# Optimization experiments

Measured on AMD Instinct MI355X. Metric: run time of the kernel, lower is better.

The kernel has to match this reference:

```python
import jax, jax.numpy as jnp
import numpy as np

NEG_SLOPE = 0.2  # PyG GATConv default


def gat_layer(x, W, att_src, att_dst, bias, src, dst, concat):
    # x: [N, F_in]; W: [F_in, H*C]; att_src/att_dst: [H, C]; bias: [H*C] or [C]
    N = x.shape[0]
    H, C = att_src.shape
    h = (x @ W).reshape(N, H, C)                       # [N, H, C]
    a_s = jnp.einsum('nhc,hc->nh', h, att_src)         # [N, H]
    a_d = jnp.einsum('nhc,hc->nh', h, att_dst)
    e = jax.nn.leaky_relu(a_s[src] + a_d[dst], NEG_SLOPE)  # [E, H]
    # segment softmax over incoming edges of each destination node
    m = jax.ops.segment_max(e, dst, num_segments=N)
    m = jnp.where(jnp.isfinite(m), m, 0.0)
    ee = jnp.exp(e - m[dst])
    s = jax.ops.segment_sum(ee, dst, num_segments=N)
    alpha = ee / (s[dst] + 1e-16)                      # [E, H]
    out = jax.ops.segment_sum(h[src] * alpha[:, :, None], dst, num_segments=N)  # [N, H, C]
    out = out.reshape(N, H * C) if concat else out.mean(axis=1)
    return out + bias


def setup_inputs() -> dict:
    key = jax.random.key(0)
    ks = jax.random.split(key, 16)
    N, E, F_IN, NC = 100000, 3200000, 256, 40
    H, C = 8, 8  # hidden GATConv: heads=8, out=8 -> width 64
    inp = {}
    inp['features'] = jax.random.normal(ks[0], (N, F_IN), dtype=jnp.float32)
    inp['edge_index'] = jax.random.randint(ks[1], (2, E), 0, N, dtype=jnp.int64)
    def p(k, shape):
        return jax.random.normal(k, shape, dtype=jnp.float32) * 0.1
    # layer 0: in 256 -> 8 heads x 8 (concat -> 64)
    inp['W0'] = p(ks[2], (F_IN, H * C)); inp['as0'] = p(ks[3], (H, C)); inp['ad0'] = p(ks[4], (H, C)); inp['b0'] = jnp.zeros((H * C,), jnp.float32)
    # layer 1: 64 -> 8 heads x 8 (concat -> 64)
    inp['W1'] = p(ks[5], (H * C, H * C)); inp['as1'] = p(ks[6], (H, C)); inp['ad1'] = p(ks[7], (H, C)); inp['b1'] = jnp.zeros((H * C,), jnp.float32)
    # layer 2: 64 -> 1 head x n_classes (mean/no-concat)
    inp['W2'] = p(ks[8], (H * C, NC)); inp['as2'] = p(ks[9], (1, NC)); inp['ad2'] = p(ks[10], (1, NC)); inp['b2'] = jnp.zeros((NC,), jnp.float32)
    return inp


def reference(features, edge_index, W0, as0, ad0, b0, W1, as1, ad1, b1, W2, as2, ad2, b2):
    N = features.shape[0]
    loops = jnp.arange(N, dtype=edge_index.dtype)  # PyG GATConv adds self-loops by default
    src = jnp.concatenate([edge_index[0], loops])
    dst = jnp.concatenate([edge_index[1], loops])
    x = gat_layer(features, W0, as0, ad0, b0, src, dst, True)
    x = gat_layer(x, W1, as1, ad1, b1, src, dst, True)
    x = gat_layer(x, W2, as2, ad2, b2, src, dst, False)
    return jax.nn.log_softmax(x, axis=-1)
```

## Files before the change

kernel.cpp:

```cpp
#include <hip/hip_runtime.h>
#include <hip/hip_bf16.h>

#define NEG_SLOPE 0.2f
#define LOG2E 1.44269504f
#define EPB 4096

typedef __attribute__((ext_vector_type(8))) short short8;
typedef __attribute__((ext_vector_type(4))) float f32x4;

__device__ __forceinline__ unsigned short f2bf(float x) {
    unsigned u = __float_as_uint(x);
    unsigned r = (u + 0x7FFFu + ((u >> 16) & 1u)) >> 16;
    return (unsigned short)r;
}

__device__ __forceinline__ float fexp2(float x) {
    return __builtin_amdgcn_exp2f(x);
}

__device__ __forceinline__ float readlane_f(float v, int l) {
    return __int_as_float(__builtin_amdgcn_readlane(__float_as_int(v), l));
}


__global__ __launch_bounds__(256) void bucket_hist_k(
    const int* __restrict__ dsts, int* __restrict__ bcnt, int E, int Etot,
    int nbuck) {
    __shared__ int lh[512];
    for (int i = threadIdx.x; i < nbuck; i += 256) lh[i] = 0;
    __syncthreads();
    int base = blockIdx.x * EPB;
    int cnt = Etot - base;
    if (cnt > EPB) cnt = EPB;
    for (int i = threadIdx.x; i < cnt; i += 256) {
        int e = base + i;
        int d = (e < E) ? dsts[e] : (e - E);
        atomicAdd(&lh[d >> 8], 1);
    }
    __syncthreads();
    for (int i = threadIdx.x; i < nbuck; i += 256) {
        int c = lh[i];
        if (c) atomicAdd(&bcnt[i], c);
    }
}

__global__ __launch_bounds__(512) void bucket_scan_k(
    const int* __restrict__ bcnt, int* __restrict__ bptr,
    int* __restrict__ bcur, int nbuck, int Etot) {
    __shared__ int tmp[512];
    int t = threadIdx.x;
    int v = (t < nbuck) ? bcnt[t] : 0;
    tmp[t] = v;
    __syncthreads();
    for (int off = 1; off < 512; off <<= 1) {
        int x = (t >= off) ? tmp[t - off] : 0;
        __syncthreads();
        tmp[t] += x;
        __syncthreads();
    }
    int excl = tmp[t] - v;
    if (t < nbuck) { bptr[t] = excl; bcur[t] = excl; }
    if (t == 0) bptr[nbuck] = Etot;
}

__global__ __launch_bounds__(256) void bucket_scatter_k(
    const int* __restrict__ srcs, const int* __restrict__ dsts,
    int* __restrict__ bcur, int2* __restrict__ pairs, int E, int Etot,
    int nbuck) {
    __shared__ int lh[512];
    __shared__ int lbase[512];
    for (int i = threadIdx.x; i < nbuck; i += 256) lh[i] = 0;
    __syncthreads();
    int base = blockIdx.x * EPB;
    int cnt = Etot - base;
    if (cnt > EPB) cnt = EPB;
    for (int i = threadIdx.x; i < cnt; i += 256) {
        int e = base + i;
        int d = (e < E) ? dsts[e] : (e - E);
        atomicAdd(&lh[d >> 8], 1);
    }
    __syncthreads();
    for (int i = threadIdx.x; i < nbuck; i += 256) {
        int c = lh[i];
        lbase[i] = c ? atomicAdd(&bcur[i], c) : 0;
    }
    __syncthreads();
    for (int i = threadIdx.x; i < nbuck; i += 256) lh[i] = 0;
    __syncthreads();
    for (int i = threadIdx.x; i < cnt; i += 256) {
        int e = base + i;
        int s, d;
        if (e < E) { s = srcs[e]; d = dsts[e]; }
        else       { s = e - E;   d = s; }
        int b = d >> 8;
        int off = atomicAdd(&lh[b], 1);
        pairs[lbase[b] + off] = make_int2(s, d);
    }
}

__global__ __launch_bounds__(256) void bucket_sort_k(
    const int2* __restrict__ pairs, const int* __restrict__ bptr,
    int* __restrict__ row_ptr, int* __restrict__ csr_src, int N, int Etot,
    int nbuck) {
    __shared__ int lh[256];
    __shared__ int lscan[256];
    int b = blockIdx.x;
    int n0 = b << 8;
    int e0 = bptr[b], e1 = bptr[b + 1];
    int t = threadIdx.x;
    lh[t] = 0;
    __syncthreads();
    for (int e = e0 + t; e < e1; e += 256)
        atomicAdd(&lh[pairs[e].y - n0], 1);
    __syncthreads();
    int v = lh[t];
    lscan[t] = v;
    __syncthreads();
    for (int off = 1; off < 256; off <<= 1) {
        int x = (t >= off) ? lscan[t - off] : 0;
        __syncthreads();
        lscan[t] += x;
        __syncthreads();
    }
    int start = e0 + lscan[t] - v;
    int n = n0 + t;
    if (n < N) row_ptr[n] = start;
    lh[t] = start;
    __syncthreads();
    for (int e = e0 + t; e < e1; e += 256) {
        int2 p = pairs[e];
        int pos = atomicAdd(&lh[p.y - n0], 1);
        csr_src[pos] = p.x;
    }
    if (b == nbuck - 1 && t == 0) row_ptr[N] = Etot;
}


template <int K>
__global__ __launch_bounds__(256) void gemm_pack8_k(
    const float* __restrict__ x, const float* __restrict__ W,
    const float* __restrict__ a_src, const float* __restrict__ a_dst,
    char* __restrict__ hrec, float* __restrict__ asb,
    float* __restrict__ adb, int N) {
    constexpr int NT = 4;
    constexpr int KT = K / 32;
    constexpr size_t WF_BYTES = (size_t)KT * NT * 64 * 8 * sizeof(short);
    constexpr size_t H_BYTES = (size_t)64 * 65 * sizeof(float);
    __shared__ alignas(16) char smem[WF_BYTES > H_BYTES ? WF_BYTES : H_BYTES];
    short* Wf = (short*)smem;
    float* hL = (float*)smem;
    int tid = threadIdx.x;
    for (int f = tid; f < KT * NT * 64; f += 256) {
        int lane = f & 63;
        int ntk = f >> 6;
        int nt = ntk % NT, kt = ntk / NT;
        int q = lane >> 4, c = lane & 15;
        int n = nt * 16 + c;
        int k0 = kt * 32 + q * 8;
        short8 frag;
        #pragma unroll
        for (int j = 0; j < 8; ++j)
            frag[j] = (short)f2bf(W[(size_t)(k0 + j) * 64 + n]);
        *(short8*)&Wf[f * 8] = frag;
    }
    __syncthreads();
    int wave = tid >> 6, lane = tid & 63;
    int q = lane >> 4, c = lane & 15;
    int m0 = blockIdx.x * 64 + wave * 16;
    int arow = m0 + c;
    int arl = arow < N ? arow : N - 1;
    f32x4 acc[NT] = {};
    for (int kt = 0; kt < KT; ++kt) {
        const float* xp = x + (size_t)arl * K + kt * 32 + q * 8;
        float4 a0 = *(const float4*)xp;
        float4 a1 = *(const float4*)(xp + 4);
        float av[8] = {a0.x, a0.y, a0.z, a0.w, a1.x, a1.y, a1.z, a1.w};
        short8 af;
        #pragma unroll
        for (int j = 0; j < 8; ++j) af[j] = (short)f2bf(av[j]);
        #pragma unroll
        for (int nt = 0; nt < NT; ++nt) {
            short8 bf = *(const short8*)&Wf[((kt * NT + nt) * 64 + lane) * 8];
            acc[nt] = __builtin_amdgcn_mfma_f32_16x16x32_bf16(af, bf, acc[nt],
                                                              0, 0, 0);
        }
    }
    __syncthreads();
    int lrow = wave * 16 + q * 4;
    #pragma unroll
    for (int nt = 0; nt < NT; ++nt)
        #pragma unroll
        for (int reg = 0; reg < 4; ++reg)
            hL[(lrow + reg) * 65 + nt * 16 + c] = acc[nt][reg];
    __syncthreads();
    #pragma unroll
    for (int it = 0; it < 2; ++it) {
        int id = it * 256 + tid;
        int ln = id >> 3, hd = id & 7;
        int gn = blockIdx.x * 64 + ln;
        if (gn >= N) continue;
        const float* hp = &hL[ln * 65 + hd * 8];
        float as = 0.f, ad = 0.f;
        float hv[8];
        #pragma unroll
        for (int j = 0; j < 8; ++j) {
            hv[j] = hp[j];
            as += hv[j] * a_src[hd * 8 + j];
            ad += hv[j] * a_dst[hd * 8 + j];
        }
        adb[gn * 8 + hd] = ad * LOG2E;
        asb[gn * 8 + hd] = as * LOG2E;
        unsigned short u[8];
        #pragma unroll
        for (int j = 0; j < 8; ++j) u[j] = f2bf(hv[j]);
        uint4 pk;
        pk.x = (unsigned)u[0] | ((unsigned)u[1] << 16);
        pk.y = (unsigned)u[2] | ((unsigned)u[3] << 16);
        pk.z = (unsigned)u[4] | ((unsigned)u[5] << 16);
        pk.w = (unsigned)u[6] | ((unsigned)u[7] << 16);
        *(uint4*)(hrec + (size_t)gn * 128 + hd * 16) = pk;
    }
}


__global__ __launch_bounds__(256) void gemm_pack40_k(
    const float* __restrict__ x, const float* __restrict__ W,
    const float* __restrict__ a_src, const float* __restrict__ a_dst,
    char* __restrict__ h40, float* __restrict__ asb40,
    float* __restrict__ adb, int N) {
    constexpr int K = 64, NT = 3, KT = 2;
    constexpr size_t WF_BYTES = (size_t)KT * NT * 64 * 8 * sizeof(short);
    constexpr size_t H_BYTES = (size_t)64 * 41 * sizeof(float);
    __shared__ alignas(16) char smem[WF_BYTES > H_BYTES ? WF_BYTES : H_BYTES];
    short* Wf = (short*)smem;
    float* hL = (float*)smem;
    int tid = threadIdx.x;
    for (int f = tid; f < KT * NT * 64; f += 256) {
        int lane = f & 63;
        int ntk = f >> 6;
        int nt = ntk % NT, kt = ntk / NT;
        int q = lane >> 4, c = lane & 15;
        int n = nt * 16 + c;
        int k0 = kt * 32 + q * 8;
        short8 frag;
        #pragma unroll
        for (int j = 0; j < 8; ++j) {
            float v = (n < 40) ? W[(size_t)(k0 + j) * 40 + n] : 0.f;
            frag[j] = (short)f2bf(v);
        }
        *(short8*)&Wf[f * 8] = frag;
    }
    __syncthreads();
    int wave = tid >> 6, lane = tid & 63;
    int q = lane >> 4, c = lane & 15;
    int m0 = blockIdx.x * 64 + wave * 16;
    int arow = m0 + c;
    int arl = arow < N ? arow : N - 1;
    f32x4 acc[NT] = {};
    for (int kt = 0; kt < KT; ++kt) {
        const float* xp = x + (size_t)arl * K + kt * 32 + q * 8;
        float4 a0 = *(const float4*)xp;
        float4 a1 = *(const float4*)(xp + 4);
        float av[8] = {a0.x, a0.y, a0.z, a0.w, a1.x, a1.y, a1.z, a1.w};
        short8 af;
        #pragma unroll
        for (int j = 0; j < 8; ++j) af[j] = (short)f2bf(av[j]);
        #pragma unroll
        for (int nt = 0; nt < NT; ++nt) {
            short8 bf = *(const short8*)&Wf[((kt * NT + nt) * 64 + lane) * 8];
            acc[nt] = __builtin_amdgcn_mfma_f32_16x16x32_bf16(af, bf, acc[nt],
                                                              0, 0, 0);
        }
    }
    __syncthreads();
    int lrow = wave * 16 + q * 4;
    #pragma unroll
    for (int nt = 0; nt < NT; ++nt) {
        int n = nt * 16 + c;
        if (n >= 40) continue;
        #pragma unroll
        for (int reg = 0; reg < 4; ++reg)
            hL[(lrow + reg) * 41 + n] = acc[nt][reg];
    }
    __syncthreads();
    int ln = tid >> 2, sub = tid & 3;
    int gn = blockIdx.x * 64 + ln;
    float pas = 0.f, pad = 0.f;
    if (gn < N) {
        for (int j = sub; j < 40; j += 4) {
            float hv = hL[ln * 41 + j];
            pas += hv * a_src[j];
            pad += hv * a_dst[j];
        }
    }
    pas += __shfl_xor(pas, 1); pas += __shfl_xor(pas, 2);
    pad += __shfl_xor(pad, 1); pad += __shfl_xor(pad, 2);
    if (gn < N && sub == 0) {
        asb40[gn] = pas * LOG2E;
        adb[gn] = pad * LOG2E;
    }
    for (int i = tid; i < 64 * 40; i += 256) {
        int n2 = i / 40, ch = i % 40;
        int g2 = blockIdx.x * 64 + n2;
        if (g2 < N)
            *(unsigned short*)(h40 + (size_t)g2 * 80 + ch * 2) =
                f2bf(hL[n2 * 41 + ch]);
    }
}


#define EDGE64(SUF, IDX)                                                     \
    int s##SUF = __builtin_amdgcn_readlane(sv, (IDX));                       \
    float w##SUF = lwp[(IDX)];                                               \
    unsigned u##SUF =                                                        \
        *(const unsigned short*)(hrec + (size_t)s##SUF * 128 + lane2);

__global__ __launch_bounds__(256) void aggr64_k(
    const char* __restrict__ hrec, const float* __restrict__ asb,
    const float* __restrict__ adb, const int* __restrict__ row_ptr,
    const int* __restrict__ csr_src, const float* __restrict__ bias,
    float* __restrict__ out, int N) {
    __shared__ float wlds[4 * 1040];
    int wave = threadIdx.x >> 6;
    int node = blockIdx.x * 4 + wave;
    if (node >= N) return;
    int lane = threadIdx.x & 63;
    int hd = lane >> 3;
    int lane2 = lane * 2;
    float* wbA = wlds + wave * 1040;
    float* wbB = wbA + 520;
    const float* lwpA = wbA + hd * 65;
    const float* lwpB = wbB + hd * 65;
    int beg = row_ptr[node], end = row_ptr[node + 1];
    float4 adv0 = *(const float4*)(adb + (size_t)node * 8);
    float4 adv1 = *(const float4*)(adb + (size_t)node * 8 + 4);
    float acc0 = 0.f, acc1 = 0.f, acc2 = 0.f, acc3 = 0.f;
    float acc4 = 0.f, acc5 = 0.f, acc6 = 0.f, acc7 = 0.f;
    float l0 = 0.f, l1 = 0.f, l2 = 0.f, l3 = 0.f;
    float l4 = 0.f, l5 = 0.f, l6 = 0.f, l7 = 0.f;
    int par = 0;
    for (int i0 = beg; i0 < end; i0 += 64, par ^= 1) {
        int tail = end - i0;
        int sv = csr_src[i0 + (lane < tail ? lane : 0)];
        int cnt = tail < 64 ? tail : 64;
        float* wb = par ? wbB : wbA;
        const float* lwp = par ? lwpB : lwpA;
        {
            const float* asp = asb + (size_t)sv * 8;
            float4 s0 = *(const float4*)asp;
            float4 s1 = *(const float4*)(asp + 4);
            float w0 = s0.x + adv0.x; w0 = fmaxf(w0, NEG_SLOPE * w0); w0 = fexp2(w0);
            float w1 = s0.y + adv0.y; w1 = fmaxf(w1, NEG_SLOPE * w1); w1 = fexp2(w1);
            float w2 = s0.z + adv0.z; w2 = fmaxf(w2, NEG_SLOPE * w2); w2 = fexp2(w2);
            float w3 = s0.w + adv0.w; w3 = fmaxf(w3, NEG_SLOPE * w3); w3 = fexp2(w3);
            float w4 = s1.x + adv1.x; w4 = fmaxf(w4, NEG_SLOPE * w4); w4 = fexp2(w4);
            float w5 = s1.y + adv1.y; w5 = fmaxf(w5, NEG_SLOPE * w5); w5 = fexp2(w5);
            float w6 = s1.z + adv1.z; w6 = fmaxf(w6, NEG_SLOPE * w6); w6 = fexp2(w6);
            float w7 = s1.w + adv1.w; w7 = fmaxf(w7, NEG_SLOPE * w7); w7 = fexp2(w7);
            wb[lane]       = w0;
            wb[65 + lane]  = w1;
            wb[130 + lane] = w2;
            wb[195 + lane] = w3;
            wb[260 + lane] = w4;
            wb[325 + lane] = w5;
            wb[390 + lane] = w6;
            wb[455 + lane] = w7;
        }
        int j = 0;
        for (; j + 8 <= cnt; j += 8) {
            EDGE64(A, j)      EDGE64(B, j + 1) EDGE64(C, j + 2) EDGE64(D, j + 3)
            EDGE64(E2, j + 4) EDGE64(F, j + 5) EDGE64(G, j + 6) EDGE64(H2, j + 7)
            l0 += wA; l1 += wB; l2 += wC; l3 += wD;
            l4 += wE2; l5 += wF; l6 += wG; l7 += wH2;
            acc0 = fmaf(wA, __uint_as_float(uA << 16), acc0);
            acc1 = fmaf(wB, __uint_as_float(uB << 16), acc1);
            acc2 = fmaf(wC, __uint_as_float(uC << 16), acc2);
            acc3 = fmaf(wD, __uint_as_float(uD << 16), acc3);
            acc4 = fmaf(wE2, __uint_as_float(uE2 << 16), acc4);
            acc5 = fmaf(wF, __uint_as_float(uF << 16), acc5);
            acc6 = fmaf(wG, __uint_as_float(uG << 16), acc6);
            acc7 = fmaf(wH2, __uint_as_float(uH2 << 16), acc7);
        }
        for (; j + 4 <= cnt; j += 4) {
            EDGE64(A, j) EDGE64(B, j + 1) EDGE64(C, j + 2) EDGE64(D, j + 3)
            l0 += wA; l1 += wB; l2 += wC; l3 += wD;
            acc0 = fmaf(wA, __uint_as_float(uA << 16), acc0);
            acc1 = fmaf(wB, __uint_as_float(uB << 16), acc1);
            acc2 = fmaf(wC, __uint_as_float(uC << 16), acc2);
            acc3 = fmaf(wD, __uint_as_float(uD << 16), acc3);
        }
        for (; j < cnt; ++j) {
            EDGE64(A, j)
            l0 += wA;
            acc0 = fmaf(wA, __uint_as_float(uA << 16), acc0);
        }
    }
    float l = ((l0 + l1) + (l2 + l3)) + ((l4 + l5) + (l6 + l7));
    float acc = ((acc0 + acc1) + (acc2 + acc3)) + ((acc4 + acc5) + (acc6 + acc7));
    out[(size_t)node * 64 + lane] = acc / (l + 1e-16f) + bias[lane];
}


#define F40(SUF, IDX)                                                        \
    int s##SUF = __builtin_amdgcn_readlane(sv, (IDX));                       \
    float w##SUF = readlane_f(wv, (IDX));                                    \
    unsigned u##SUF =                                                        \
        *(const unsigned short*)(hrec + (size_t)s##SUF * 80 + cl2);

__global__ __launch_bounds__(256) void aggr40_k(
    const char* __restrict__ hrec, const float* __restrict__ asb,
    const float* __restrict__ adb, const int* __restrict__ row_ptr,
    const int* __restrict__ csr_src, const float* __restrict__ bias,
    float* __restrict__ out, int N) {
    int node = blockIdx.x * 4 + (threadIdx.x >> 6);
    if (node >= N) return;
    int lane = threadIdx.x & 63;
    int cl2 = (lane < 40 ? lane : 0) * 2;
    int beg = row_ptr[node], end = row_ptr[node + 1];
    float ad = adb[node];
    float acc0 = 0.f, acc1 = 0.f, acc2 = 0.f, acc3 = 0.f;
    float acc4 = 0.f, acc5 = 0.f, acc6 = 0.f, acc7 = 0.f;
    float lpart = 0.f;
    for (int i0 = beg; i0 < end; i0 += 64) {
        int tail = end - i0;
        int sv = csr_src[i0 + (lane < tail ? lane : 0)];
        int cnt = tail < 64 ? tail : 64;
        float as = asb[sv];
        float v = as + ad;
        v = fmaxf(v, NEG_SLOPE * v);
        float wv = fexp2(v);
        wv = (lane < cnt) ? wv : 0.f;
        lpart += wv;
        int j = 0;
        for (; j + 8 <= cnt; j += 8) {
            F40(A, j)     F40(B, j + 1) F40(C, j + 2) F40(D, j + 3)
            F40(E2, j + 4) F40(F, j + 5) F40(G, j + 6) F40(H2, j + 7)
            acc0 = fmaf(wA, __uint_as_float(uA << 16), acc0);
            acc1 = fmaf(wB, __uint_as_float(uB << 16), acc1);
            acc2 = fmaf(wC, __uint_as_float(uC << 16), acc2);
            acc3 = fmaf(wD, __uint_as_float(uD << 16), acc3);
            acc4 = fmaf(wE2, __uint_as_float(uE2 << 16), acc4);
            acc5 = fmaf(wF, __uint_as_float(uF << 16), acc5);
            acc6 = fmaf(wG, __uint_as_float(uG << 16), acc6);
            acc7 = fmaf(wH2, __uint_as_float(uH2 << 16), acc7);
        }
        for (; j + 4 <= cnt; j += 4) {
            F40(A, j) F40(B, j + 1) F40(C, j + 2) F40(D, j + 3)
            acc0 = fmaf(wA, __uint_as_float(uA << 16), acc0);
            acc1 = fmaf(wB, __uint_as_float(uB << 16), acc1);
            acc2 = fmaf(wC, __uint_as_float(uC << 16), acc2);
            acc3 = fmaf(wD, __uint_as_float(uD << 16), acc3);
        }
        for (; j < cnt; ++j) {
            F40(A, j)
            acc0 = fmaf(wA, __uint_as_float(uA << 16), acc0);
        }
    }
    #pragma unroll
    for (int off = 32; off > 0; off >>= 1) lpart += __shfl_xor(lpart, off);
    float l = lpart;
    float acc = ((acc0 + acc1) + (acc2 + acc3)) + ((acc4 + acc5) + (acc6 + acc7));
    float val = acc / (l + 1e-16f) + ((lane < 40) ? bias[lane] : 0.f);
    float mval = (lane < 40) ? val : -1e30f;
    #pragma unroll
    for (int off = 32; off > 0; off >>= 1)
        mval = fmaxf(mval, __shfl_xor(mval, off));
    float ex = (lane < 40) ? __expf(val - mval) : 0.f;
    #pragma unroll
    for (int off = 32; off > 0; off >>= 1) ex += __shfl_xor(ex, off);
    if (lane < 40)
        out[(size_t)node * 40 + lane] = val - mval - __logf(ex);
}


extern "C" void kernel_launch(void* const* d_in, const int* in_sizes, int n_in,
                              void* d_out, int out_size, void* d_ws,
                              size_t ws_size, hipStream_t stream) {
    const float* features = (const float*)d_in[0];
    const int* edge_index = (const int*)d_in[1];
    const float* W0 = (const float*)d_in[2];
    const float* as0 = (const float*)d_in[3];
    const float* ad0 = (const float*)d_in[4];
    const float* b0 = (const float*)d_in[5];
    const float* W1 = (const float*)d_in[6];
    const float* as1 = (const float*)d_in[7];
    const float* ad1 = (const float*)d_in[8];
    const float* b1 = (const float*)d_in[9];
    const float* W2 = (const float*)d_in[10];
    const float* as2 = (const float*)d_in[11];
    const float* ad2 = (const float*)d_in[12];
    const float* b2 = (const float*)d_in[13];

    int N = in_sizes[0] / 256;
    int E = in_sizes[1] / 2;
    int Etot = E + N;
    int nbuck = (N + 255) >> 8;
    const int* srcs = edge_index;
    const int* dsts = edge_index + E;

    float* ws = (float*)d_ws;
    float* Hbuf = ws;
    float* Abuf = Hbuf + (size_t)N * 64;
    float* adb  = Abuf + (size_t)N * 64;
    float* asb  = adb + (size_t)N * 8;
    char* hrec  = (char*)(asb + (size_t)N * 8);
    int* row_ptr = (int*)(hrec + (size_t)N * 128);
    int* bcnt    = row_ptr + (N + 2);
    int* bptr    = bcnt + 512;
    int* bcur    = bptr + 513;
    int* csr_src = bcur + 512;
    int2* pairs  = (int2*)Hbuf;

    const int B = 256;
    int gAg = (N + 3) / 4;
    int gBk = (Etot + EPB - 1) / EPB;
    int gGm = (N + 63) / 64;

    (void)hipMemsetAsync(bcnt, 0, 512 * 4, stream);
    bucket_hist_k<<<gBk, B, 0, stream>>>(dsts, bcnt, E, Etot, nbuck);
    bucket_scan_k<<<1, 512, 0, stream>>>(bcnt, bptr, bcur, nbuck, Etot);
    bucket_scatter_k<<<gBk, B, 0, stream>>>(srcs, dsts, bcur, pairs, E, Etot,
                                            nbuck);
    bucket_sort_k<<<nbuck, B, 0, stream>>>(pairs, bptr, row_ptr, csr_src, N,
                                           Etot, nbuck);

    gemm_pack8_k<256><<<gGm, B, 0, stream>>>(features, W0, as0, ad0, hrec,
                                             asb, adb, N);
    aggr64_k<<<gAg, B, 0, stream>>>(hrec, asb, adb, row_ptr, csr_src, b0,
                                    Abuf, N);

    gemm_pack8_k<64><<<gGm, B, 0, stream>>>(Abuf, W1, as1, ad1, hrec, asb,
                                            adb, N);
    aggr64_k<<<gAg, B, 0, stream>>>(hrec, asb, adb, row_ptr, csr_src, b1,
                                    Abuf, N);

    gemm_pack40_k<<<gGm, B, 0, stream>>>(Abuf, W2, as2, ad2, hrec, asb, adb,
                                         N);
    aggr40_k<<<gAg, B, 0, stream>>>(hrec, asb, adb, row_ptr, csr_src, b2,
                                    (float*)d_out, N);
}
```

Measured before the change: 622.8 us.

## Build CSR with global per-node atomic degree count and direct scatter

Replaces the two-level bucket sort (bucket histogram, bucket scatter of int2 pairs, per-bucket LDS sort) with a per-node degree count via global atomics, a three-kernel prefix scan that also places each self-loop first in its row, and a direct atomic scatter of source ids into csr_src. This drops the intermediate pairs buffer and one full pass over the edges. In exchange it relies on 3.2M scattered global atomics twice, and neighbour order within a row becomes nondeterministic, which can change floating-point summation order.

```diff
diff --git a/kernel.cpp b/kernel.cpp
--- a/kernel.cpp
+++ b/kernel.cpp
@@ -3,7 +3,6 @@
 
 #define NEG_SLOPE 0.2f
 #define LOG2E 1.44269504f
-#define EPB 4096
 
 typedef __attribute__((ext_vector_type(8))) short short8;
 typedef __attribute__((ext_vector_type(4))) float f32x4;
@@ -23,33 +22,46 @@
 }
 
 
-__global__ __launch_bounds__(256) void bucket_hist_k(
-    const int* __restrict__ dsts, int* __restrict__ bcnt, int E, int Etot,
-    int nbuck) {
-    __shared__ int lh[512];
-    for (int i = threadIdx.x; i < nbuck; i += 256) lh[i] = 0;
-    __syncthreads();
-    int base = blockIdx.x * EPB;
-    int cnt = Etot - base;
-    if (cnt > EPB) cnt = EPB;
-    for (int i = threadIdx.x; i < cnt; i += 256) {
-        int e = base + i;
-        int d = (e < E) ? dsts[e] : (e - E);
-        atomicAdd(&lh[d >> 8], 1);
-    }
-    __syncthreads();
-    for (int i = threadIdx.x; i < nbuck; i += 256) {
-        int c = lh[i];
-        if (c) atomicAdd(&bcnt[i], c);
-    }
-}
-
-__global__ __launch_bounds__(512) void bucket_scan_k(
-    const int* __restrict__ bcnt, int* __restrict__ bptr,
-    int* __restrict__ bcur, int nbuck, int Etot) {
+__global__ __launch_bounds__(256) void deg_count_k(
+    const int* __restrict__ dsts, int* __restrict__ deg, int E) {
+    int tid = blockIdx.x * 256 + threadIdx.x;
+    int stride = gridDim.x * 256;
+    if ((E & 3) == 0) {
+        int nq = E >> 2;
+        const int4* d4p = (const int4*)dsts;
+        for (int i = tid; i < nq; i += stride) {
+            int4 d = d4p[i];
+            atomicAdd(&deg[d.x], 1);
+            atomicAdd(&deg[d.y], 1);
+            atomicAdd(&deg[d.z], 1);
+            atomicAdd(&deg[d.w], 1);
+        }
+    } else {
+        for (int e = tid; e < E; e += stride) atomicAdd(&deg[dsts[e]], 1);
+    }
+}
+
+__global__ __launch_bounds__(256) void scan_part_k(
+    const int* __restrict__ deg, int* __restrict__ bsum, int N) {
+    int b = blockIdx.x;
+    int n = b * 256 + threadIdx.x;
+    int v = (n < N) ? deg[n] + 1 : 0;
+    #pragma unroll
+    for (int off = 32; off > 0; off >>= 1) v += __shfl_xor(v, off);
+    __shared__ int wsum[4];
+    int lane = threadIdx.x & 63, wave = threadIdx.x >> 6;
+    if (lane == 0) wsum[wave] = v;
+    __syncthreads();
+    if (threadIdx.x == 0)
+        bsum[b] = wsum[0] + wsum[1] + wsum[2] + wsum[3];
+}
+
+__global__ __launch_bounds__(512) void scan_top_k(
+    const int* __restrict__ bsum, int* __restrict__ bbase,
+    int* __restrict__ row_ptr, int NB, int N, int Etot) {
     __shared__ int tmp[512];
     int t = threadIdx.x;
-    int v = (t < nbuck) ? bcnt[t] : 0;
+    int v = (t < NB) ? bsum[t] : 0;
     tmp[t] = v;
     __syncthreads();
     for (int off = 1; off < 512; off <<= 1) {
@@ -58,81 +70,62 @@
         tmp[t] += x;
         __syncthreads();
     }
-    int excl = tmp[t] - v;
-    if (t < nbuck) { bptr[t] = excl; bcur[t] = excl; }
-    if (t == 0) bptr[nbuck] = Etot;
-}
-
-__global__ __launch_bounds__(256) void bucket_scatter_k(
+    if (t < NB) bbase[t] = tmp[t] - v;
+    if (t == 0) row_ptr[N] = Etot;
+}
+
+__global__ __launch_bounds__(256) void scan_write_k(
+    const int* __restrict__ deg, const int* __restrict__ bbase,
+    int* __restrict__ row_ptr, int* __restrict__ csr_src,
+    int* __restrict__ cur, int N) {
+    __shared__ int tmp[256];
+    int b = blockIdx.x;
+    int t = threadIdx.x;
+    int n = b * 256 + t;
+    int v = (n < N) ? deg[n] + 1 : 0;
+    tmp[t] = v;
+    __syncthreads();
+    for (int off = 1; off < 256; off <<= 1) {
+        int x = (t >= off) ? tmp[t - off] : 0;
+        __syncthreads();
+        tmp[t] += x;
+        __syncthreads();
+    }
+    if (n < N) {
+        int rp = bbase[b] + tmp[t] - v;
+        row_ptr[n] = rp;
+        csr_src[rp] = n;
+        cur[n] = rp + 1;
+    }
+}
+
+__global__ __launch_bounds__(256) void scatter_k(
     const int* __restrict__ srcs, const int* __restrict__ dsts,
-    int* __restrict__ bcur, int2* __restrict__ pairs, int E, int Etot,
-    int nbuck) {
-    __shared__ int lh[512];
-    __shared__ int lbase[512];
-    for (int i = threadIdx.x; i < nbuck; i += 256) lh[i] = 0;
-    __syncthreads();
-    int base = blockIdx.x * EPB;
-    int cnt = Etot - base;
-    if (cnt > EPB) cnt = EPB;
-    for (int i = threadIdx.x; i < cnt; i += 256) {
-        int e = base + i;
-        int d = (e < E) ? dsts[e] : (e - E);
-        atomicAdd(&lh[d >> 8], 1);
-    }
-    __syncthreads();
-    for (int i = threadIdx.x; i < nbuck; i += 256) {
-        int c = lh[i];
-        lbase[i] = c ? atomicAdd(&bcur[i], c) : 0;
-    }
-    __syncthreads();
-    for (int i = threadIdx.x; i < nbuck; i += 256) lh[i] = 0;
-    __syncthreads();
-    for (int i = threadIdx.x; i < cnt; i += 256) {
-        int e = base + i;
-        int s, d;
-        if (e < E) { s = srcs[e]; d = dsts[e]; }
-        else       { s = e - E;   d = s; }
-        int b = d >> 8;
-        int off = atomicAdd(&lh[b], 1);
-        pairs[lbase[b] + off] = make_int2(s, d);
-    }
-}
-
-__global__ __launch_bounds__(256) void bucket_sort_k(
-    const int2* __restrict__ pairs, const int* __restrict__ bptr,
-    int* __restrict__ row_ptr, int* __restrict__ csr_src, int N, int Etot,
-    int nbuck) {
-    __shared__ int lh[256];
-    __shared__ int lscan[256];
-    int b = blockIdx.x;
-    int n0 = b << 8;
-    int e0 = bptr[b], e1 = bptr[b + 1];
-    int t = threadIdx.x;
-    lh[t] = 0;
-    __syncthreads();
-    for (int e = e0 + t; e < e1; e += 256)
-        atomicAdd(&lh[pairs[e].y - n0], 1);
-    __syncthreads();
-    int v = lh[t];
-    lscan[t] = v;
-    __syncthreads();
-    for (int off = 1; off < 256; off <<= 1) {
-        int x = (t >= off) ? lscan[t - off] : 0;
-        __syncthreads();
-        lscan[t] += x;
-        __syncthreads();
-    }
-    int start = e0 + lscan[t] - v;
-    int n = n0 + t;
-    if (n < N) row_ptr[n] = start;
-    lh[t] = start;
-    __syncthreads();
-    for (int e = e0 + t; e < e1; e += 256) {
-        int2 p = pairs[e];
-        int pos = atomicAdd(&lh[p.y - n0], 1);
-        csr_src[pos] = p.x;
-    }
-    if (b == nbuck - 1 && t == 0) row_ptr[N] = Etot;
+    int* __restrict__ cur, int* __restrict__ csr_src, int E) {
+    int tid = blockIdx.x * 256 + threadIdx.x;
+    int stride = gridDim.x * 256;
+    if ((E & 3) == 0) {
+        int nq = E >> 2;
+        const int4* s4p = (const int4*)srcs;
+        const int4* d4p = (const int4*)dsts;
+        for (int i = tid; i < nq; i += stride) {
+            int4 s = s4p[i];
+            int4 d = d4p[i];
+            int p0 = atomicAdd(&cur[d.x], 1);
+            int p1 = atomicAdd(&cur[d.y], 1);
+            int p2 = atomicAdd(&cur[d.z], 1);
+            int p3 = atomicAdd(&cur[d.w], 1);
+            csr_src[p0] = s.x;
+            csr_src[p1] = s.y;
+            csr_src[p2] = s.z;
+            csr_src[p3] = s.w;
+        }
+    } else {
+        for (int e = tid; e < E; e += stride) {
+            int p = atomicAdd(&cur[dsts[e]], 1);
+            csr_src[p] = srcs[e];
+        }
+    }
 }
 
 
@@ -494,7 +487,7 @@
     int N = in_sizes[0] / 256;
     int E = in_sizes[1] / 2;
     int Etot = E + N;
-    int nbuck = (N + 255) >> 8;
+    int NB = (N + 255) >> 8;
     const int* srcs = edge_index;
     const int* dsts = edge_index + E;
 
@@ -505,24 +498,25 @@
     float* asb  = adb + (size_t)N * 8;
     char* hrec  = (char*)(asb + (size_t)N * 8);
     int* row_ptr = (int*)(hrec + (size_t)N * 128);
-    int* bcnt    = row_ptr + (N + 2);
-    int* bptr    = bcnt + 512;
-    int* bcur    = bptr + 513;
-    int* csr_src = bcur + 512;
-    int2* pairs  = (int2*)Hbuf;
+    int* deg     = row_ptr + (N + 2);
+    int* cur     = deg + N;
+    int* bsum    = cur + N;
+    int* bbase   = bsum + 512;
+    int* csr_src = bbase + 512;
 
     const int B = 256;
     int gAg = (N + 3) / 4;
-    int gBk = (Etot + EPB - 1) / EPB;
     int gGm = (N + 63) / 64;
-
-    (void)hipMemsetAsync(bcnt, 0, 512 * 4, stream);
-    bucket_hist_k<<<gBk, B, 0, stream>>>(dsts, bcnt, E, Etot, nbuck);
-    bucket_scan_k<<<1, 512, 0, stream>>>(bcnt, bptr, bcur, nbuck, Etot);
-    bucket_scatter_k<<<gBk, B, 0, stream>>>(srcs, dsts, bcur, pairs, E, Etot,
-                                            nbuck);
-    bucket_sort_k<<<nbuck, B, 0, stream>>>(pairs, bptr, row_ptr, csr_src, N,
-                                           Etot, nbuck);
+    int nq = (E + 3) >> 2;
+    int gEd = (nq + 255) / 256;
+    if (gEd > 8192) gEd = 8192;
+
+    (void)hipMemsetAsync(deg, 0, (size_t)N * 4, stream);
+    deg_count_k<<<gEd, B, 0, stream>>>(dsts, deg, E);
+    scan_part_k<<<NB, B, 0, stream>>>(deg, bsum, N);
+    scan_top_k<<<1, 512, 0, stream>>>(bsum, bbase, row_ptr, NB, N, Etot);
+    scan_write_k<<<NB, B, 0, stream>>>(deg, bbase, row_ptr, csr_src, cur, N);
+    scatter_k<<<gEd, B, 0, stream>>>(srcs, dsts, cur, csr_src, E);
 
     gemm_pack8_k<256><<<gGm, B, 0, stream>>>(features, W0, as0, ad0, hrec,
                                              asb, adb, N);
```

After: 907.0 us. 1.46x slower.

## Restructure CSR build: packed pairs, cached histograms, implicit self-loops, finer buckets

Applied to the files above, without the earlier changes.

The edge bucketing pipeline is reworked. Each block's per-bucket histogram is saved so the scatter pass no longer recounts, and src and low dst bits are packed into one int instead of an int2. Self-loops are inserted analytically in the sort stage rather than scattered, and buckets shrink from 256 to 128 nodes with vectorized int4 edge loads and larger blocks. The aim is to cut memory traffic and atomic work in CSR construction, at the cost of an extra bhist buffer and a src<<7 packing that needs src under 2^24.

```diff
diff --git a/kernel.cpp b/kernel.cpp
--- a/kernel.cpp
+++ b/kernel.cpp
@@ -3,7 +3,8 @@
 
 #define NEG_SLOPE 0.2f
 #define LOG2E 1.44269504f
-#define EPB 4096
+#define EPB 8192
+#define MAXBUCK 800
 
 typedef __attribute__((ext_vector_type(8))) short short8;
 typedef __attribute__((ext_vector_type(4))) float f32x4;
@@ -24,115 +25,143 @@
 
 
 __global__ __launch_bounds__(256) void bucket_hist_k(
-    const int* __restrict__ dsts, int* __restrict__ bcnt, int E, int Etot,
-    int nbuck) {
-    __shared__ int lh[512];
-    for (int i = threadIdx.x; i < nbuck; i += 256) lh[i] = 0;
+    const int* __restrict__ dsts, int* __restrict__ bcnt,
+    int* __restrict__ bhist, int E, int nbuck) {
+    __shared__ int lh[MAXBUCK];
+    int t = threadIdx.x;
+    for (int i = t; i < nbuck; i += 256) lh[i] = 0;
     __syncthreads();
     int base = blockIdx.x * EPB;
-    int cnt = Etot - base;
+    int cnt = E - base;
     if (cnt > EPB) cnt = EPB;
-    for (int i = threadIdx.x; i < cnt; i += 256) {
-        int e = base + i;
-        int d = (e < E) ? dsts[e] : (e - E);
-        atomicAdd(&lh[d >> 8], 1);
-    }
-    __syncthreads();
-    for (int i = threadIdx.x; i < nbuck; i += 256) {
+    int nq = cnt >> 2;
+    const int4* d4p = (const int4*)(dsts + base);
+    for (int i = t; i < nq; i += 256) {
+        int4 d = d4p[i];
+        atomicAdd(&lh[d.x >> 7], 1);
+        atomicAdd(&lh[d.y >> 7], 1);
+        atomicAdd(&lh[d.z >> 7], 1);
+        atomicAdd(&lh[d.w >> 7], 1);
+    }
+    for (int i = (nq << 2) + t; i < cnt; i += 256)
+        atomicAdd(&lh[dsts[base + i] >> 7], 1);
+    __syncthreads();
+    int* bh = bhist + (size_t)blockIdx.x * MAXBUCK;
+    for (int i = t; i < nbuck; i += 256) {
         int c = lh[i];
+        bh[i] = c;
         if (c) atomicAdd(&bcnt[i], c);
     }
 }
 
 __global__ __launch_bounds__(512) void bucket_scan_k(
-    const int* __restrict__ bcnt, int* __restrict__ bptr,
-    int* __restrict__ bcur, int nbuck, int Etot) {
-    __shared__ int tmp[512];
+    const int* __restrict__ bcnt, int* __restrict__ bptrE,
+    int* __restrict__ bcurE, int nbuck) {
+    __shared__ int csum[512];
     int t = threadIdx.x;
-    int v = (t < nbuck) ? bcnt[t] : 0;
-    tmp[t] = v;
+    int i0 = t * 4;
+    int v0 = 0, v1 = 0, v2 = 0, v3 = 0;
+    if (i0 < nbuck) v0 = bcnt[i0];
+    if (i0 + 1 < nbuck) v1 = bcnt[i0 + 1];
+    if (i0 + 2 < nbuck) v2 = bcnt[i0 + 2];
+    if (i0 + 3 < nbuck) v3 = bcnt[i0 + 3];
+    int s = v0 + v1 + v2 + v3;
+    csum[t] = s;
     __syncthreads();
     for (int off = 1; off < 512; off <<= 1) {
-        int x = (t >= off) ? tmp[t - off] : 0;
+        int x = (t >= off) ? csum[t - off] : 0;
         __syncthreads();
-        tmp[t] += x;
+        csum[t] += x;
         __syncthreads();
     }
-    int excl = tmp[t] - v;
-    if (t < nbuck) { bptr[t] = excl; bcur[t] = excl; }
-    if (t == 0) bptr[nbuck] = Etot;
-}
-
-__global__ __launch_bounds__(256) void bucket_scatter_k(
+    int base = csum[t] - s;
+    if (i0 < nbuck)     { bptrE[i0] = base;     bcurE[i0] = base; }     base += v0;
+    if (i0 + 1 < nbuck) { bptrE[i0 + 1] = base; bcurE[i0 + 1] = base; } base += v1;
+    if (i0 + 2 < nbuck) { bptrE[i0 + 2] = base; bcurE[i0 + 2] = base; } base += v2;
+    if (i0 + 3 < nbuck) { bptrE[i0 + 3] = base; bcurE[i0 + 3] = base; }
+}
+
+__global__ __launch_bounds__(256) void bscatter_k(
     const int* __restrict__ srcs, const int* __restrict__ dsts,
-    int* __restrict__ bcur, int2* __restrict__ pairs, int E, int Etot,
-    int nbuck) {
-    __shared__ int lh[512];
-    __shared__ int lbase[512];
-    for (int i = threadIdx.x; i < nbuck; i += 256) lh[i] = 0;
+    const int* __restrict__ bhist, int* __restrict__ bcurE,
+    int* __restrict__ pairs, int E, int nbuck) {
+    __shared__ int lh[MAXBUCK];
+    __shared__ int lbase[MAXBUCK];
+    int t = threadIdx.x;
+    const int* bh = bhist + (size_t)blockIdx.x * MAXBUCK;
+    for (int i = t; i < nbuck; i += 256) {
+        int c = bh[i];
+        lbase[i] = c ? atomicAdd(&bcurE[i], c) : 0;
+        lh[i] = 0;
+    }
     __syncthreads();
     int base = blockIdx.x * EPB;
-    int cnt = Etot - base;
+    int cnt = E - base;
     if (cnt > EPB) cnt = EPB;
-    for (int i = threadIdx.x; i < cnt; i += 256) {
-        int e = base + i;
-        int d = (e < E) ? dsts[e] : (e - E);
-        atomicAdd(&lh[d >> 8], 1);
-    }
-    __syncthreads();
-    for (int i = threadIdx.x; i < nbuck; i += 256) {
-        int c = lh[i];
-        lbase[i] = c ? atomicAdd(&bcur[i], c) : 0;
-    }
-    __syncthreads();
-    for (int i = threadIdx.x; i < nbuck; i += 256) lh[i] = 0;
-    __syncthreads();
-    for (int i = threadIdx.x; i < cnt; i += 256) {
-        int e = base + i;
-        int s, d;
-        if (e < E) { s = srcs[e]; d = dsts[e]; }
-        else       { s = e - E;   d = s; }
-        int b = d >> 8;
-        int off = atomicAdd(&lh[b], 1);
-        pairs[lbase[b] + off] = make_int2(s, d);
+    int nq = cnt >> 2;
+    const int4* d4p = (const int4*)(dsts + base);
+    const int4* s4p = (const int4*)(srcs + base);
+    for (int i = t; i < nq; i += 256) {
+        int4 d = d4p[i];
+        int4 s = s4p[i];
+        int b0 = d.x >> 7, b1 = d.y >> 7, b2 = d.z >> 7, b3 = d.w >> 7;
+        int r0 = atomicAdd(&lh[b0], 1);
+        int r1 = atomicAdd(&lh[b1], 1);
+        int r2 = atomicAdd(&lh[b2], 1);
+        int r3 = atomicAdd(&lh[b3], 1);
+        pairs[lbase[b0] + r0] = (s.x << 7) | (d.x & 127);
+        pairs[lbase[b1] + r1] = (s.y << 7) | (d.y & 127);
+        pairs[lbase[b2] + r2] = (s.z << 7) | (d.z & 127);
+        pairs[lbase[b3] + r3] = (s.w << 7) | (d.w & 127);
+    }
+    for (int i = (nq << 2) + t; i < cnt; i += 256) {
+        int s = srcs[base + i], d = dsts[base + i];
+        int r = atomicAdd(&lh[d >> 7], 1);
+        pairs[lbase[d >> 7] + r] = (s << 7) | (d & 127);
     }
 }
 
 __global__ __launch_bounds__(256) void bucket_sort_k(
-    const int2* __restrict__ pairs, const int* __restrict__ bptr,
-    int* __restrict__ row_ptr, int* __restrict__ csr_src, int N, int Etot,
-    int nbuck) {
-    __shared__ int lh[256];
-    __shared__ int lscan[256];
+    const int* __restrict__ pairs, const int* __restrict__ bptrE,
+    const int* __restrict__ bcurE, int* __restrict__ row_ptr,
+    int* __restrict__ csr_src, int N, int Etot) {
+    __shared__ int lh[128];
+    __shared__ int sc[128];
     int b = blockIdx.x;
-    int n0 = b << 8;
-    int e0 = bptr[b], e1 = bptr[b + 1];
+    int n0 = b << 7;
     int t = threadIdx.x;
-    lh[t] = 0;
-    __syncthreads();
+    if (t < 128) lh[t] = 0;
+    __syncthreads();
+    int e0 = bptrE[b], e1 = bcurE[b];
     for (int e = e0 + t; e < e1; e += 256)
-        atomicAdd(&lh[pairs[e].y - n0], 1);
-    __syncthreads();
-    int v = lh[t];
-    lscan[t] = v;
-    __syncthreads();
-    for (int off = 1; off < 256; off <<= 1) {
-        int x = (t >= off) ? lscan[t - off] : 0;
+        atomicAdd(&lh[pairs[e] & 127], 1);
+    __syncthreads();
+    if (t < 128) sc[t] = lh[t];
+    __syncthreads();
+    for (int off = 1; off < 128; off <<= 1) {
+        int x = (t < 128 && t >= off) ? sc[t - off] : 0;
         __syncthreads();
-        lscan[t] += x;
+        if (t < 128) sc[t] += x;
         __syncthreads();
     }
-    int start = e0 + lscan[t] - v;
-    int n = n0 + t;
-    if (n < N) row_ptr[n] = start;
-    lh[t] = start;
+    if (t < 128) {
+        int cntv = lh[t];
+        int excl = sc[t] - cntv;
+        int n = n0 + t;
+        int rp = e0 + n0 + t + excl;
+        if (n < N) {
+            row_ptr[n] = rp;
+            csr_src[rp] = n;
+        }
+        lh[t] = rp + 1;
+    }
     __syncthreads();
     for (int e = e0 + t; e < e1; e += 256) {
-        int2 p = pairs[e];
-        int pos = atomicAdd(&lh[p.y - n0], 1);
-        csr_src[pos] = p.x;
-    }
-    if (b == nbuck - 1 && t == 0) row_ptr[N] = Etot;
+        int p = pairs[e];
+        int pos = atomicAdd(&lh[p & 127], 1);
+        csr_src[pos] = p >> 7;
+    }
+    if (b == 0 && t == 0) row_ptr[N] = Etot;
 }
 
 
@@ -405,10 +434,10 @@
     int s##SUF = __builtin_amdgcn_readlane(sv, (IDX));                       \
     float w##SUF = readlane_f(wv, (IDX));                                    \
     unsigned u##SUF =                                                        \
-        *(const unsigned short*)(hrec + (size_t)s##SUF * 80 + cl2);
+        *(const unsigned short*)(rec40 + (size_t)s##SUF * 80 + cl2);
 
 __global__ __launch_bounds__(256) void aggr40_k(
-    const char* __restrict__ hrec, const float* __restrict__ asb,
+    const char* __restrict__ rec40, const float* __restrict__ asb,
     const float* __restrict__ adb, const int* __restrict__ row_ptr,
     const int* __restrict__ csr_src, const float* __restrict__ bias,
     float* __restrict__ out, int N) {
@@ -494,7 +523,7 @@
     int N = in_sizes[0] / 256;
     int E = in_sizes[1] / 2;
     int Etot = E + N;
-    int nbuck = (N + 255) >> 8;
+    int nbuck = (N + 127) >> 7;
     const int* srcs = edge_index;
     const int* dsts = edge_index + E;
 
@@ -506,23 +535,24 @@
     char* hrec  = (char*)(asb + (size_t)N * 8);
     int* row_ptr = (int*)(hrec + (size_t)N * 128);
     int* bcnt    = row_ptr + (N + 2);
-    int* bptr    = bcnt + 512;
-    int* bcur    = bptr + 513;
-    int* csr_src = bcur + 512;
-    int2* pairs  = (int2*)Hbuf;
+    int* bptrE   = bcnt + MAXBUCK;
+    int* bcurE   = bptrE + MAXBUCK;
+    int* csr_src = bcurE + MAXBUCK;
+    int* bhist   = csr_src + Etot;
+    int* pairs   = (int*)Hbuf;
 
     const int B = 256;
     int gAg = (N + 3) / 4;
-    int gBk = (Etot + EPB - 1) / EPB;
     int gGm = (N + 63) / 64;
-
-    (void)hipMemsetAsync(bcnt, 0, 512 * 4, stream);
-    bucket_hist_k<<<gBk, B, 0, stream>>>(dsts, bcnt, E, Etot, nbuck);
-    bucket_scan_k<<<1, 512, 0, stream>>>(bcnt, bptr, bcur, nbuck, Etot);
-    bucket_scatter_k<<<gBk, B, 0, stream>>>(srcs, dsts, bcur, pairs, E, Etot,
-                                            nbuck);
-    bucket_sort_k<<<nbuck, B, 0, stream>>>(pairs, bptr, row_ptr, csr_src, N,
-                                           Etot, nbuck);
+    int gSc = (E + EPB - 1) / EPB;
+
+    (void)hipMemsetAsync(bcnt, 0, MAXBUCK * 4, stream);
+    bucket_hist_k<<<gSc, B, 0, stream>>>(dsts, bcnt, bhist, E, nbuck);
+    bucket_scan_k<<<1, 512, 0, stream>>>(bcnt, bptrE, bcurE, nbuck);
+    bscatter_k<<<gSc, B, 0, stream>>>(srcs, dsts, bhist, bcurE, pairs, E,
+                                      nbuck);
+    bucket_sort_k<<<nbuck, B, 0, stream>>>(pairs, bptrE, bcurE, row_ptr,
+                                           csr_src, N, Etot);
 
     gemm_pack8_k<256><<<gGm, B, 0, stream>>>(features, W0, as0, ad0, hrec,
                                              asb, adb, N);
```

New measurement: 579.6 us. -6.9%, faster.
